# Kernel optimization log

Measured on AMD Instinct MI355X. Metric: run time of the kernel, lower is better.

Reference implementation:

```python
import jax, jax.numpy as jnp
import numpy as np

BETA = 0.85
THRESHOLD = 1.0
T, B = 1000, 256
N_IN, N_HID, N_OUT = 3, 200, 1


def setup_inputs() -> dict:
    key = jax.random.key(0)
    k0, k1, k2, k3 = jax.random.split(key, 4)
    inputs = jax.random.normal(k0, (T, B, N_IN), dtype=jnp.float32)
    # Learned parameters (nn.Linear weights are [out, in]; snntorch RLeaky
    # all_to_all recurrent is a Linear(N_HID, N_HID) with bias).
    W1 = jax.random.normal(k1, (N_HID, N_IN), dtype=jnp.float32) * 0.3
    b1 = jnp.zeros((N_HID,), jnp.float32)
    Wrec = jax.random.normal(k2, (N_HID, N_HID), dtype=jnp.float32) * 0.05
    brec = jnp.zeros((N_HID,), jnp.float32)
    W2 = jax.random.normal(k3, (N_OUT, N_HID), dtype=jnp.float32) * 0.1
    b2 = jnp.zeros((N_OUT,), jnp.float32)
    return dict(inputs=inputs, W1=W1, b1=b1, Wrec=Wrec, brec=brec, W2=W2, b2=b2)


def reference(inputs, W1, b1, Wrec, brec, W2, b2):
    # RLeaky (snntorch) with zero reset:
    #   reset   = heaviside(mem_prev - threshold)          (from old mem)
    #   base    = beta*mem_prev + cur1 + Wrec@spk_prev + brec
    #   mem_new = base - reset * base
    #   spk_new = heaviside(mem_new - threshold)
    batch = inputs.shape[1]
    nhid = W1.shape[0]

    def step(carry, x_t):
        spk, mem = carry
        cur1 = x_t @ W1.T + b1                      # [B, N_HID]
        base = BETA * mem + cur1 + spk @ Wrec.T + brec
        reset = (mem > THRESHOLD).astype(mem.dtype)
        mem_new = base - reset * base               # zero reset
        spk_new = (mem_new > THRESHOLD).astype(mem.dtype)
        cur2 = spk_new @ W2.T + b2                  # [B, N_OUT]
        return (spk_new, mem_new), (cur2, spk_new)

    init = (jnp.zeros((batch, nhid), inputs.dtype),
            jnp.zeros((batch, nhid), inputs.dtype))
    _, (cur2_rec, spk1_rec) = jax.lax.scan(step, init, inputs)
    return cur2_rec, spk1_rec  # [T,B,1], [T,B,200]
```

## Files before the change

kernel.cpp:

```cpp
#include <hip/hip_runtime.h>

#define T_STEPS 1000
#define BATCH   256
#define NHID    200
#define ROWF    200
#define BETA_C  0.85f
#define THR_C   1.0f


#define BARRIER_LGKM \
    asm volatile("s_waitcnt lgkmcnt(0)\n\ts_barrier" ::: "memory");

__launch_bounds__(256, 1)
__global__ void rsnn_kernel(const float* __restrict__ X,
                            const float* __restrict__ W1,
                            const float* __restrict__ b1,
                            const float* __restrict__ Wrec,
                            const float* __restrict__ brec,
                            float* __restrict__ out_spk) {
#pragma clang fp contract(off)
    __shared__ float WT2[NHID * ROWF];
    __shared__ float part[4][4][50];

    const int tid = threadIdx.x;
    const int l   = tid & 63;
    const int w   = tid >> 6;
    const int b   = blockIdx.x;

    for (int idx = tid; idx < NHID * NHID; idx += 256) {
        int r  = idx / NHID;
        int i  = idx - r * NHID;
        int lo = r % 50, k = r / 50;
        WT2[i * ROWF + lo * 4 + k] = Wrec[idx];
    }
    __syncthreads();

    const int lc = (l < 50) ? l : 49;
    const int oc = 50 * w + lc;
    const float w10 = W1[oc * 3 + 0], w11 = W1[oc * 3 + 1], w12 = W1[oc * 3 + 2];
    const float b1j = b1[oc], brj = brec[oc];

    float mem = 0.f;
    unsigned long long bm = 0;

    const float* xp = X + (size_t)b * 3;

    const float* ldsrow  = WT2 + (size_t)lc * 4;
    const int    wbase   = 50 * w;
    float*       spk_out = out_spk + (size_t)b * NHID + wbase + lc;

    float xc[8][3];
#pragma unroll
    for (int k = 0; k < 8; ++k) {
        xc[k][0] = xp[(size_t)k * (BATCH * 3) + 0];
        xc[k][1] = xp[(size_t)k * (BATCH * 3) + 1];
        xc[k][2] = xp[(size_t)k * (BATCH * 3) + 2];
    }

#define REC_WORD(MASK, BASE)                                                          \
    {                                                                                 \
        unsigned long long m = (MASK);                                                \
        while (m) {                                                                   \
            int i0 = __builtin_ctzll(m); m &= m - 1;                                  \
            bool h1 = m != 0; int i1 = h1 ? __builtin_ctzll(m) : i0; if (h1) m &= m - 1; \
            bool h2 = m != 0; int i2 = h2 ? __builtin_ctzll(m) : i0; if (h2) m &= m - 1; \
            bool h3 = m != 0; int i3 = h3 ? __builtin_ctzll(m) : i0; if (h3) m &= m - 1; \
            const float4 v0 = *(const float4*)(ldsrow + (i0 + (BASE)) * ROWF);        \
            const float4 v1 = *(const float4*)(ldsrow + (i1 + (BASE)) * ROWF);        \
            const float4 v2 = *(const float4*)(ldsrow + (i2 + (BASE)) * ROWF);        \
            const float4 v3 = *(const float4*)(ldsrow + (i3 + (BASE)) * ROWF);        \
            pr0 += v0.x; pr1 += v0.y; pr2 += v0.z; pr3 += v0.w;                       \
            if (h1) { pr0 += v1.x; pr1 += v1.y; pr2 += v1.z; pr3 += v1.w; }           \
            if (h2) { pr0 += v2.x; pr1 += v2.y; pr2 += v2.z; pr3 += v2.w; }           \
            if (h3) { pr0 += v3.x; pr1 += v3.y; pr2 += v3.z; pr3 += v3.w; }           \
        }                                                                             \
    }

#define STEP(T, K)                                                       \
    {                                                                    \
        const int t = (T);                                               \
                                                                         \
        float pr0 = 0.f, pr1 = 0.f, pr2 = 0.f, pr3 = 0.f;                \
        REC_WORD(bm, wbase)                                              \
                                                                         \
        if (l < 50) {                                                    \
            part[0][w][l] = pr0;                                         \
            part[1][w][l] = pr1;                                         \
            part[2][w][l] = pr2;                                         \
            part[3][w][l] = pr3;                                         \
        }                                                                \
        BARRIER_LGKM                                                     \
                                                                         \
        float p0 = part[w][0][lc], p1 = part[w][1][lc];                  \
        float p2 = part[w][2][lc], p3 = part[w][3][lc];                  \
        float rec = ((p0 + p1) + p2) + p3;                               \
        BARRIER_LGKM                                                     \
                                                                         \
        float c1 = fmaf(xc[K][2], w12,                                   \
                        fmaf(xc[K][1], w11, xc[K][0] * w10)) + b1j;      \
        float ba = ((BETA_C * mem + c1) + rec) + brj;                    \
        float nm = (mem > THR_C) ? 0.f : ba;                             \
        float sp = (nm > THR_C) ? 1.f : 0.f;                             \
        mem = nm;                                                        \
                                                                         \
        if (l < 50)                                                      \
            spk_out[(size_t)t * BATCH * NHID] = sp;                      \
        bm = __ballot((l < 50) && (sp > 0.5f));                          \
    }

    for (int g = 0; g < T_STEPS; g += 8) {
        const int gn = (g + 8 < T_STEPS) ? g + 8 : 0;
        float xn[8][3];
#pragma unroll
        for (int k = 0; k < 8; ++k) {
            xn[k][0] = xp[(size_t)(gn + k) * (BATCH * 3) + 0];
            xn[k][1] = xp[(size_t)(gn + k) * (BATCH * 3) + 1];
            xn[k][2] = xp[(size_t)(gn + k) * (BATCH * 3) + 2];
        }

        STEP(g + 0, 0)
        STEP(g + 1, 1)
        STEP(g + 2, 2)
        STEP(g + 3, 3)
        STEP(g + 4, 4)
        STEP(g + 5, 5)
        STEP(g + 6, 6)
        STEP(g + 7, 7)

#pragma unroll
        for (int k = 0; k < 8; ++k) {
            xc[k][0] = xn[k][0];
            xc[k][1] = xn[k][1];
            xc[k][2] = xn[k][2];
        }
    }
#undef STEP
#undef REC_WORD
}

__launch_bounds__(256)
__global__ void cur2_kernel(const float* __restrict__ spk,
                            const float* __restrict__ W2,
                            const float* __restrict__ b2,
                            float* __restrict__ out) {
    const int lane = threadIdx.x & 63;
    const int wid  = (int)((blockIdx.x * blockDim.x + threadIdx.x) >> 6);
    const int nw   = (int)((gridDim.x * blockDim.x) >> 6);

    float4 w2v = {0.f, 0.f, 0.f, 0.f};
    if (lane < 50) w2v = *(const float4*)(W2 + lane * 4);
    const float b2v = b2[0];

    for (int p = wid; p < T_STEPS * BATCH; p += nw) {
        float4 sv = {0.f, 0.f, 0.f, 0.f};
        if (lane < 50) sv = *(const float4*)(spk + (size_t)p * NHID + lane * 4);
        float a = fmaf(sv.w, w2v.w, fmaf(sv.z, w2v.z,
                  fmaf(sv.y, w2v.y, sv.x * w2v.x)));
#pragma unroll
        for (int o = 32; o >= 1; o >>= 1) a += __shfl_xor(a, o);
        if (lane == 0) out[p] = a + b2v;
    }
}

extern "C" void kernel_launch(void* const* d_in, const int* in_sizes, int n_in,
                              void* d_out, int out_size, void* d_ws, size_t ws_size,
                              hipStream_t stream) {
    const float* X    = (const float*)d_in[0];
    const float* W1   = (const float*)d_in[1];
    const float* b1   = (const float*)d_in[2];
    const float* Wrec = (const float*)d_in[3];
    const float* brec = (const float*)d_in[4];
    const float* W2   = (const float*)d_in[5];
    const float* b2   = (const float*)d_in[6];

    float* out_cur2 = (float*)d_out;
    float* out_spk  = (float*)d_out + (size_t)T_STEPS * BATCH;

    rsnn_kernel<<<BATCH, 256, 0, stream>>>(X, W1, b1, Wrec, brec, out_spk);
    cur2_kernel<<<1024, 256, 0, stream>>>(out_spk, W2, b2, out_cur2);
}
```

Baseline: 509.2 us.

## Double-buffer partial sums to drop one barrier per timestep

Partial recurrent sums now alternate between two LDS buffers, so the second barrier in each step can be removed while keeping reads and writes separated. To fit the extra buffer, the last four rows of the transposed recurrent weights move out of LDS into registers for wave 3, which handles those spike bits with explicit conditional adds. This reduces synchronization on the serial time loop, at the cost of a branch on the wave index and a few extra registers.

```diff
diff --git a/kernel.cpp b/kernel.cpp
--- a/kernel.cpp
+++ b/kernel.cpp
@@ -4,6 +4,7 @@
 #define BATCH   256
 #define NHID    200
 #define ROWF    200
+#define NROWS   196
 #define BETA_C  0.85f
 #define THR_C   1.0f
 
@@ -19,8 +20,8 @@
                             const float* __restrict__ brec,
                             float* __restrict__ out_spk) {
 #pragma clang fp contract(off)
-    __shared__ float WT2[NHID * ROWF];
-    __shared__ float part[4][4][50];
+    __shared__ float WT2[NROWS * ROWF];
+    __shared__ float part[2][4][4][50];
 
     const int tid = threadIdx.x;
     const int l   = tid & 63;
@@ -28,10 +29,12 @@
     const int b   = blockIdx.x;
 
     for (int idx = tid; idx < NHID * NHID; idx += 256) {
-        int r  = idx / NHID;
-        int i  = idx - r * NHID;
-        int lo = r % 50, k = r / 50;
-        WT2[i * ROWF + lo * 4 + k] = Wrec[idx];
+        int r = idx / NHID;
+        int i = idx - r * NHID;
+        if (i < NROWS) {
+            int lo = r % 50, k = r / 50;
+            WT2[i * ROWF + lo * 4 + k] = Wrec[idx];
+        }
     }
     __syncthreads();
 
@@ -39,6 +42,15 @@
     const int oc = 50 * w + lc;
     const float w10 = W1[oc * 3 + 0], w11 = W1[oc * 3 + 1], w12 = W1[oc * 3 + 2];
     const float b1j = b1[oc], brj = brec[oc];
+
+    float4 rr[4];
+#pragma unroll
+    for (int j = 0; j < 4; ++j) {
+        rr[j].x = Wrec[(lc +   0) * NHID + NROWS + j];
+        rr[j].y = Wrec[(lc +  50) * NHID + NROWS + j];
+        rr[j].z = Wrec[(lc + 100) * NHID + NROWS + j];
+        rr[j].w = Wrec[(lc + 150) * NHID + NROWS + j];
+    }
 
     float mem = 0.f;
     unsigned long long bm = 0;
@@ -76,25 +88,37 @@
         }                                                                             \
     }
 
-#define STEP(T, K)                                                       \
+#define STEP(T, K, P)                                                    \
     {                                                                    \
         const int t = (T);                                               \
                                                                          \
         float pr0 = 0.f, pr1 = 0.f, pr2 = 0.f, pr3 = 0.f;                \
-        REC_WORD(bm, wbase)                                              \
+        if (w == 3) {                                                    \
+            unsigned long long mlo = bm & ((1ull << 46) - 1);            \
+            REC_WORD(mlo, wbase)                                         \
+            if (bm & (1ull << 46)) { pr0 += rr[0].x; pr1 += rr[0].y;     \
+                                     pr2 += rr[0].z; pr3 += rr[0].w; }   \
+            if (bm & (1ull << 47)) { pr0 += rr[1].x; pr1 += rr[1].y;     \
+                                     pr2 += rr[1].z; pr3 += rr[1].w; }   \
+            if (bm & (1ull << 48)) { pr0 += rr[2].x; pr1 += rr[2].y;     \
+                                     pr2 += rr[2].z; pr3 += rr[2].w; }   \
+            if (bm & (1ull << 49)) { pr0 += rr[3].x; pr1 += rr[3].y;     \
+                                     pr2 += rr[3].z; pr3 += rr[3].w; }   \
+        } else {                                                         \
+            REC_WORD(bm, wbase)                                          \
+        }                                                                \
                                                                          \
         if (l < 50) {                                                    \
-            part[0][w][l] = pr0;                                         \
-            part[1][w][l] = pr1;                                         \
-            part[2][w][l] = pr2;                                         \
-            part[3][w][l] = pr3;                                         \
+            part[P][0][w][l] = pr0;                                      \
+            part[P][1][w][l] = pr1;                                      \
+            part[P][2][w][l] = pr2;                                      \
+            part[P][3][w][l] = pr3;                                      \
         }                                                                \
         BARRIER_LGKM                                                     \
                                                                          \
-        float p0 = part[w][0][lc], p1 = part[w][1][lc];                  \
-        float p2 = part[w][2][lc], p3 = part[w][3][lc];                  \
+        float p0 = part[P][w][0][lc], p1 = part[P][w][1][lc];            \
+        float p2 = part[P][w][2][lc], p3 = part[P][w][3][lc];            \
         float rec = ((p0 + p1) + p2) + p3;                               \
-        BARRIER_LGKM                                                     \
                                                                          \
         float c1 = fmaf(xc[K][2], w12,                                   \
                         fmaf(xc[K][1], w11, xc[K][0] * w10)) + b1j;      \
@@ -118,14 +142,14 @@
             xn[k][2] = xp[(size_t)(gn + k) * (BATCH * 3) + 2];
         }
 
-        STEP(g + 0, 0)
-        STEP(g + 1, 1)
-        STEP(g + 2, 2)
-        STEP(g + 3, 3)
-        STEP(g + 4, 4)
-        STEP(g + 5, 5)
-        STEP(g + 6, 6)
-        STEP(g + 7, 7)
+        STEP(g + 0, 0, 0)
+        STEP(g + 1, 1, 1)
+        STEP(g + 2, 2, 0)
+        STEP(g + 3, 3, 1)
+        STEP(g + 4, 4, 0)
+        STEP(g + 5, 5, 1)
+        STEP(g + 6, 6, 0)
+        STEP(g + 7, 7, 1)
 
 #pragma unroll
         for (int k = 0; k < 8; ++k) {
```

Measured after the change: 572.0 us. 1.12x slower.

## Split recurrent spike accumulation across two wave halves per output group

Applied to the files above, without the earlier changes.

Doubles the block to 512 threads so each group of 50 output neurons is served by two waves, each handling half of the source-spike bits (25 each). This halves the serial ctz/LDS-gather loop length per wave in the recurrent matvec. Partial sums from both halves are combined through an enlarged shared buffer. To fit LDS, the last 4 source rows of Wrec are kept in registers of wave 7 instead of shared memory. The cost is more barrier participants, duplicated membrane-update work in the upper waves, and an extra partial-sum read per step.

```diff
diff --git a/kernel.cpp b/kernel.cpp
--- a/kernel.cpp
+++ b/kernel.cpp
@@ -4,6 +4,7 @@
 #define BATCH   256
 #define NHID    200
 #define ROWF    200
+#define NROWS   196
 #define BETA_C  0.85f
 #define THR_C   1.0f
 
@@ -11,7 +12,7 @@
 #define BARRIER_LGKM \
     asm volatile("s_waitcnt lgkmcnt(0)\n\ts_barrier" ::: "memory");
 
-__launch_bounds__(256, 1)
+__launch_bounds__(512, 1)
 __global__ void rsnn_kernel(const float* __restrict__ X,
                             const float* __restrict__ W1,
                             const float* __restrict__ b1,
@@ -19,19 +20,23 @@
                             const float* __restrict__ brec,
                             float* __restrict__ out_spk) {
 #pragma clang fp contract(off)
-    __shared__ float WT2[NHID * ROWF];
-    __shared__ float part[4][4][50];
+    __shared__ float WT2[NROWS * ROWF];
+    __shared__ float part[2][4][4][50];
 
     const int tid = threadIdx.x;
     const int l   = tid & 63;
-    const int w   = tid >> 6;
+    const int wv  = tid >> 6;
+    const int w   = wv & 3;
+    const int hi  = wv >> 2;
     const int b   = blockIdx.x;
 
-    for (int idx = tid; idx < NHID * NHID; idx += 256) {
-        int r  = idx / NHID;
-        int i  = idx - r * NHID;
-        int lo = r % 50, k = r / 50;
-        WT2[i * ROWF + lo * 4 + k] = Wrec[idx];
+    for (int idx = tid; idx < NHID * NHID; idx += 512) {
+        int r = idx / NHID;
+        int i = idx - r * NHID;
+        if (i < NROWS) {
+            int lo = r % 50, k = r / 50;
+            WT2[i * ROWF + lo * 4 + k] = Wrec[idx];
+        }
     }
     __syncthreads();
 
@@ -40,14 +45,24 @@
     const float w10 = W1[oc * 3 + 0], w11 = W1[oc * 3 + 1], w12 = W1[oc * 3 + 2];
     const float b1j = b1[oc], brj = brec[oc];
 
+    float4 rr[4];
+#pragma unroll
+    for (int j = 0; j < 4; ++j) {
+        rr[j].x = Wrec[(lc +   0) * NHID + NROWS + j];
+        rr[j].y = Wrec[(lc +  50) * NHID + NROWS + j];
+        rr[j].z = Wrec[(lc + 100) * NHID + NROWS + j];
+        rr[j].w = Wrec[(lc + 150) * NHID + NROWS + j];
+    }
+
     float mem = 0.f;
     unsigned long long bm = 0;
 
     const float* xp = X + (size_t)b * 3;
 
     const float* ldsrow  = WT2 + (size_t)lc * 4;
-    const int    wbase   = 50 * w;
-    float*       spk_out = out_spk + (size_t)b * NHID + wbase + lc;
+    const int    gbase   = 50 * w + 25 * hi;
+    const bool   w7      = (wv == 7);
+    float*       spk_out = out_spk + (size_t)b * NHID + 50 * w + lc;
 
     float xc[8][3];
 #pragma unroll
@@ -81,19 +96,36 @@
         const int t = (T);                                               \
                                                                          \
         float pr0 = 0.f, pr1 = 0.f, pr2 = 0.f, pr3 = 0.f;                \
-        REC_WORD(bm, wbase)                                              \
+        unsigned long long mh = hi ? (bm >> 25) : (bm & 0x1FFFFFFull);   \
+        if (w7) {     \
+            unsigned long long ml = mh & ((1ull << 21) - 1);             \
+            REC_WORD(ml, gbase)                                          \
+            if (mh & (1ull << 21)) { pr0 += rr[0].x; pr1 += rr[0].y;     \
+                                     pr2 += rr[0].z; pr3 += rr[0].w; }   \
+            if (mh & (1ull << 22)) { pr0 += rr[1].x; pr1 += rr[1].y;     \
+                                     pr2 += rr[1].z; pr3 += rr[1].w; }   \
+            if (mh & (1ull << 23)) { pr0 += rr[2].x; pr1 += rr[2].y;     \
+                                     pr2 += rr[2].z; pr3 += rr[2].w; }   \
+            if (mh & (1ull << 24)) { pr0 += rr[3].x; pr1 += rr[3].y;     \
+                                     pr2 += rr[3].z; pr3 += rr[3].w; }   \
+        } else {                                                         \
+            REC_WORD(mh, gbase)                                          \
+        }                                                                \
                                                                          \
         if (l < 50) {                                                    \
-            part[0][w][l] = pr0;                                         \
-            part[1][w][l] = pr1;                                         \
-            part[2][w][l] = pr2;                                         \
-            part[3][w][l] = pr3;                                         \
+            part[hi][0][w][l] = pr0;                                     \
+            part[hi][1][w][l] = pr1;                                     \
+            part[hi][2][w][l] = pr2;                                     \
+            part[hi][3][w][l] = pr3;                                     \
         }                                                                \
         BARRIER_LGKM                                                     \
                                                                          \
-        float p0 = part[w][0][lc], p1 = part[w][1][lc];                  \
-        float p2 = part[w][2][lc], p3 = part[w][3][lc];                  \
-        float rec = ((p0 + p1) + p2) + p3;                               \
+        float p0l = part[0][w][0][lc], p0h = part[1][w][0][lc];          \
+        float p1l = part[0][w][1][lc], p1h = part[1][w][1][lc];          \
+        float p2l = part[0][w][2][lc], p2h = part[1][w][2][lc];          \
+        float p3l = part[0][w][3][lc], p3h = part[1][w][3][lc];          \
+        float rec = (((p0l + p0h) + (p1l + p1h))                         \
+                     + (p2l + p2h)) + (p3l + p3h);                       \
         BARRIER_LGKM                                                     \
                                                                          \
         float c1 = fmaf(xc[K][2], w12,                                   \
@@ -103,7 +135,7 @@
         float sp = (nm > THR_C) ? 1.f : 0.f;                             \
         mem = nm;                                                        \
                                                                          \
-        if (l < 50)                                                      \
+        if (hi == 0 && l < 50)                                           \
             spk_out[(size_t)t * BATCH * NHID] = sp;                      \
         bm = __ballot((l < 50) && (sp > 0.5f));                          \
     }
@@ -176,6 +208,6 @@
     float* out_cur2 = (float*)d_out;
     float* out_spk  = (float*)d_out + (size_t)T_STEPS * BATCH;
 
-    rsnn_kernel<<<BATCH, 256, 0, stream>>>(X, W1, b1, Wrec, brec, out_spk);
+    rsnn_kernel<<<BATCH, 512, 0, stream>>>(X, W1, b1, Wrec, brec, out_spk);
     cur2_kernel<<<1024, 256, 0, stream>>>(out_spk, W2, b2, out_cur2);
 }
```

After: 696.6 us. 36.8% more time.
